# Performance work log

Measured on AMD Instinct MI355X. Metric: run time of the kernel, lower is better.

The kernel has to match this reference:

```python
import jax, jax.numpy as jnp
import numpy as np

B, T, S, D, K = 512, 49, 200, 512, 128


def setup_inputs() -> dict:
    key = jax.random.key(0)
    ks = jax.random.split(key, 8)
    return {
        "ifeature": jax.random.normal(ks[0], (B, T, D), dtype=jnp.float32),
        "tfeature_h": jax.random.normal(ks[1], (B, S, D), dtype=jnp.float32),
        "w_Dense_Vi_0": jax.random.normal(ks[2], (D, K), dtype=jnp.float32) * 0.05,
        "w_Dense_Vt_0": jax.random.normal(ks[3], (D, K), dtype=jnp.float32) * 0.05,
        "w_Dense_Pi_0": jax.random.normal(ks[4], (2 * K, 1), dtype=jnp.float32) * 0.05,
        "b_Dense_Pi_0": jnp.zeros((T,), dtype=jnp.float32),
        "w_Dense_Vi_1": jax.random.normal(ks[5], (D, K), dtype=jnp.float32) * 0.05,
        "w_Dense_Vt_1": jax.random.normal(ks[6], (D, K), dtype=jnp.float32) * 0.05,
        "w_Dense_Pi_1": jax.random.normal(ks[7], (2 * K, 1), dtype=jnp.float32) * 0.05,
        "b_Dense_Pi_1": jnp.zeros((S,), dtype=jnp.float32),
    }


def reference(ifeature, tfeature_h, w_Dense_Vi_0, w_Dense_Vt_0, w_Dense_Pi_0,
              b_Dense_Pi_0, w_Dense_Vi_1, w_Dense_Vt_1, w_Dense_Pi_1, b_Dense_Pi_1):
    # tfeature: mean-pooled text, [B, D]
    tfeature = jnp.mean(tfeature_h, axis=1)

    # --- attention over image regions (title_len) ---
    w_Vi_0 = jnp.einsum('btd,dk->btk', ifeature, w_Dense_Vi_0)          # [B,T,K]
    w_Vt_0 = (tfeature @ w_Dense_Vt_0)[:, None, :]                      # [B,1,K] broadcast to T
    Hi = jnp.tanh(jnp.concatenate(
        [w_Vi_0, jnp.broadcast_to(w_Vt_0, w_Vi_0.shape)], axis=-1))     # [B,T,2K]
    Hi_w_b = jnp.einsum('btk,k->bt', Hi, w_Dense_Pi_0[:, 0]) + b_Dense_Pi_0
    Pi = jax.nn.softmax(Hi_w_b, axis=-1)                                # [B,T]
    Vi = jnp.einsum('bt,btd->bd', Pi, ifeature)                         # attended image feature

    # --- attention over text tokens (seq_len) ---
    w_Vi_1 = (Vi @ w_Dense_Vi_1)[:, None, :]                            # [B,1,K]
    w_Vt_1 = jnp.einsum('bsd,dk->bsk', tfeature_h, w_Dense_Vt_1)        # [B,S,K]
    Ht = jnp.tanh(jnp.concatenate(
        [jnp.broadcast_to(w_Vi_1, w_Vt_1.shape), w_Vt_1], axis=-1))     # [B,S,2K]
    Ht_b = jnp.einsum('bsk,k->bs', Ht, w_Dense_Pi_1[:, 0]) + b_Dense_Pi_1
    Pt = jax.nn.softmax(Ht_b, axis=-1)                                  # [B,S]

    # NOTE: original call() returns Pt_Vt (weighted tokens), not the pooled Vt.
    Pt_Vt = Pt[:, :, None] * tfeature_h                                 # [B,S,D]
    return Pt_Vt
```

## Files before the change

kernel.cpp:

```cpp
#include <hip/hip_runtime.h>
#include <math.h>

#define BB 512
#define SS 200
#define DD 512
#define KK 128
#define RR (BB * SS)

typedef __attribute__((ext_vector_type(8))) short bf16x8;
typedef __attribute__((ext_vector_type(4))) float f32x4;

__device__ inline unsigned short f2bf(float f) {
    union { float f; unsigned int u; } v; v.f = f;
    unsigned int r = v.u + 0x7FFFu + ((v.u >> 16) & 1u);
    return (unsigned short)(r >> 16);
}

__device__ inline bf16x8 pack8(const float4& a, const float4& b) {
    bf16x8 p;
    p[0] = (short)f2bf(a.x); p[1] = (short)f2bf(a.y);
    p[2] = (short)f2bf(a.z); p[3] = (short)f2bf(a.w);
    p[4] = (short)f2bf(b.x); p[5] = (short)f2bf(b.y);
    p[6] = (short)f2bf(b.z); p[7] = (short)f2bf(b.w);
    return p;
}

__device__ inline float fast_tanh(float x) {
    x = fminf(10.f, fmaxf(-10.f, x));
    float t = exp2f(x * 2.885390081777927f);
    return (t - 1.f) * __builtin_amdgcn_rcpf(t + 1.f);
}

__global__ void wt_kernel(const float* __restrict__ W, unsigned short* __restrict__ Wt2) {
    int i = blockIdx.x * 256 + threadIdx.x;
    int j = i & 7;
    int l = (i >> 3) & 63;
    int n = (i >> 9) & 7;
    int t = i >> 12;
    int k = n * 16 + (l & 15);
    int d = t * 32 + (l >> 4) * 8 + j;
    Wt2[i] = f2bf(W[d * KK + k]);
}

__global__ __launch_bounds__(256, 3) void logits_kernel(
    const float* __restrict__ tfh,
    const unsigned short* __restrict__ Wt2,
    const float* __restrict__ wpk,
    const float* __restrict__ bias,
    float* __restrict__ logits)
{
    int tid = threadIdx.x;
    int w   = tid >> 6;
    int l   = tid & 63;
    int l15 = l & 15;
    int g   = l >> 4;
    int W   = blockIdx.x * 4 + w;
    int row = W * 16 + l15;

    const float* a = tfh + (size_t)row * DD + g * 8;
    const unsigned short* bp = Wt2 + (size_t)l * 8;

    bf16x8 abf[16];
    #pragma unroll
    for (int t = 0; t < 16; ++t) {
        float4 v0 = *(const float4*)(a + t * 32);
        float4 v1 = *(const float4*)(a + t * 32 + 4);
        abf[t] = pack8(v0, v1);
    }

    f32x4 acc[8];
    #pragma unroll
    for (int n = 0; n < 8; ++n) acc[n] = (f32x4){0.f, 0.f, 0.f, 0.f};

    #pragma unroll
    for (int t = 0; t < 16; ++t) {
        const unsigned short* bt = bp + (size_t)t * (8 * 64 * 8);
        #pragma unroll
        for (int n = 0; n < 8; ++n) {
            bf16x8 bf = *(const bf16x8*)(bt + n * 512);
            acc[n] = __builtin_amdgcn_mfma_f32_16x16x32_bf16(abf[t], bf, acc[n], 0, 0, 0);
        }
    }

    float wv[8];
    #pragma unroll
    for (int n = 0; n < 8; ++n) wv[n] = wpk[n * 16 + l15];

    float rs[4];
    #pragma unroll
    for (int r = 0; r < 4; ++r) rs[r] = 0.f;
    #pragma unroll
    for (int n = 0; n < 8; ++n)
        #pragma unroll
        for (int r = 0; r < 4; ++r)
            rs[r] += fast_tanh(acc[n][r]) * wv[n];
    #pragma unroll
    for (int r = 0; r < 4; ++r) {
        float v = rs[r];
        v += __shfl_xor(v, 1, 64);
        v += __shfl_xor(v, 2, 64);
        v += __shfl_xor(v, 4, 64);
        v += __shfl_xor(v, 8, 64);
        rs[r] = v;
    }
    if (l15 == 0) {
        #pragma unroll
        for (int r = 0; r < 4; ++r) {
            int grow = W * 16 + g * 4 + r;
            logits[grow] = rs[r] + bias[grow % SS];
        }
    }
}

__global__ __launch_bounds__(1024) void softmax_mul_kernel(
    const float* __restrict__ logits,
    const float* __restrict__ tfh,
    float* __restrict__ out)
{
    int b = blockIdx.x;
    int tid = threadIdx.x;
    __shared__ float Pt[SS];
    __shared__ float wpart[16];

    float v = (tid < SS) ? logits[(size_t)b * SS + tid] : -INFINITY;
    float m = v;
    #pragma unroll
    for (int off = 32; off > 0; off >>= 1) m = fmaxf(m, __shfl_xor(m, off, 64));
    if ((tid & 63) == 0) wpart[tid >> 6] = m;
    __syncthreads();
    m = -INFINITY;
    #pragma unroll
    for (int i = 0; i < 16; ++i) m = fmaxf(m, wpart[i]);
    float e = (tid < SS) ? expf(v - m) : 0.f;
    float ssum = e;
    #pragma unroll
    for (int off = 32; off > 0; off >>= 1) ssum += __shfl_xor(ssum, off, 64);
    __syncthreads();
    if ((tid & 63) == 0) wpart[tid >> 6] = ssum;
    __syncthreads();
    ssum = 0.f;
    #pragma unroll
    for (int i = 0; i < 16; ++i) ssum += wpart[i];
    if (tid < SS) Pt[tid] = e / ssum;
    __syncthreads();

    const f32x4* src = (const f32x4*)(tfh + (size_t)b * SS * DD);
    f32x4*       dst = (f32x4*)(out + (size_t)b * SS * DD);
    const int n4 = SS * DD / 4;
    for (int i = tid; i < n4; i += 1024) {
        float p = Pt[i >> 7];
        f32x4 x = src[i];
        x = x * p;
        __builtin_nontemporal_store(x, dst + i);
    }
}

extern "C" void kernel_launch(void* const* d_in, const int* in_sizes, int n_in,
                              void* d_out, int out_size, void* d_ws, size_t ws_size,
                              hipStream_t stream) {
    const float* tfh   = (const float*)d_in[1];
    const float* wVt1  = (const float*)d_in[7];
    const float* wp1   = (const float*)d_in[8];
    const float* bias1 = (const float*)d_in[9];
    float* out = (float*)d_out;

    unsigned short* Wt2 = (unsigned short*)d_ws;
    float* logits = (float*)((char*)d_ws + (128 << 10));

    wt_kernel<<<(16 * 8 * 64 * 8) / 256, 256, 0, stream>>>(wVt1, Wt2);
    logits_kernel<<<RR / 64, 256, 0, stream>>>(tfh, Wt2, wp1 + KK, bias1, logits);
    softmax_mul_kernel<<<BB, 1024, 0, stream>>>(logits, tfh, out);
}
```

Measured before the change: 131.2 us.

## Stream A-operand loads per k-step to raise occupancy in logits kernel

Drops the up-front load of all sixteen bf16 A fragments into registers. Each k-step now converts the current chunk and prefetches the next one while its MFMAs run, and the launch bound rises from 3 to 8 blocks per CU. The aim is lower register pressure and more resident waves to hide global-memory latency. The trade-off is far less memory-level parallelism per wave: only one chunk is in flight instead of sixteen, and the outer loop is no longer unrolled.

```diff
diff --git a/kernel.cpp b/kernel.cpp
--- a/kernel.cpp
+++ b/kernel.cpp
@@ -42,7 +42,7 @@
     Wt2[i] = f2bf(W[d * KK + k]);
 }
 
-__global__ __launch_bounds__(256, 3) void logits_kernel(
+__global__ __launch_bounds__(256, 8) void logits_kernel(
     const float* __restrict__ tfh,
     const unsigned short* __restrict__ Wt2,
     const float* __restrict__ wpk,
@@ -54,46 +54,43 @@
     int l   = tid & 63;
     int l15 = l & 15;
     int g   = l >> 4;
-    int W   = blockIdx.x * 4 + w;
-    int row = W * 16 + l15;
+    int Wv  = blockIdx.x * 4 + w;
+    int row = Wv * 16 + l15;
 
     const float* a = tfh + (size_t)row * DD + g * 8;
     const unsigned short* bp = Wt2 + (size_t)l * 8;
-
-    bf16x8 abf[16];
-    #pragma unroll
-    for (int t = 0; t < 16; ++t) {
-        float4 v0 = *(const float4*)(a + t * 32);
-        float4 v1 = *(const float4*)(a + t * 32 + 4);
-        abf[t] = pack8(v0, v1);
-    }
 
     f32x4 acc[8];
     #pragma unroll
     for (int n = 0; n < 8; ++n) acc[n] = (f32x4){0.f, 0.f, 0.f, 0.f};
 
-    #pragma unroll
+    float4 c0 = *(const float4*)(a);
+    float4 c1 = *(const float4*)(a + 4);
+
     for (int t = 0; t < 16; ++t) {
+        bf16x8 af = pack8(c0, c1);
+        if (t < 15) {
+            c0 = *(const float4*)(a + (t + 1) * 32);
+            c1 = *(const float4*)(a + (t + 1) * 32 + 4);
+        }
         const unsigned short* bt = bp + (size_t)t * (8 * 64 * 8);
         #pragma unroll
         for (int n = 0; n < 8; ++n) {
             bf16x8 bf = *(const bf16x8*)(bt + n * 512);
-            acc[n] = __builtin_amdgcn_mfma_f32_16x16x32_bf16(abf[t], bf, acc[n], 0, 0, 0);
+            acc[n] = __builtin_amdgcn_mfma_f32_16x16x32_bf16(af, bf, acc[n], 0, 0, 0);
         }
     }
-
-    float wv[8];
-    #pragma unroll
-    for (int n = 0; n < 8; ++n) wv[n] = wpk[n * 16 + l15];
 
     float rs[4];
     #pragma unroll
     for (int r = 0; r < 4; ++r) rs[r] = 0.f;
     #pragma unroll
-    for (int n = 0; n < 8; ++n)
+    for (int n = 0; n < 8; ++n) {
+        float wv = wpk[n * 16 + l15];
         #pragma unroll
         for (int r = 0; r < 4; ++r)
-            rs[r] += fast_tanh(acc[n][r]) * wv[n];
+            rs[r] += fast_tanh(acc[n][r]) * wv;
+    }
     #pragma unroll
     for (int r = 0; r < 4; ++r) {
         float v = rs[r];
@@ -106,7 +103,7 @@
     if (l15 == 0) {
         #pragma unroll
         for (int r = 0; r < 4; ++r) {
-            int grow = W * 16 + g * 4 + r;
+            int grow = Wv * 16 + g * 4 + r;
             logits[grow] = rs[r] + bias[grow % SS];
         }
     }
```

Result: no change. 130.8 us (-0.3%).

## Split logits GEMM into two N-half passes with LDS-staged weights

Applied to the files above, without the earlier changes.

Replaces the single logits kernel with two launches of a half-width kernel. Each launch covers 64 of the 128 K columns and stages its bf16 weight slice in shared memory instead of reading it from global memory per MFMA. The second launch adds the first launch's partial sums and the bias. This halves accumulator registers and lifts the occupancy cap. In exchange, the 210 MB tfeature_h activation is read and converted to bf16 twice, which adds substantial HBM traffic to a memory-bound pipeline.

```diff
diff --git a/kernel.cpp b/kernel.cpp
--- a/kernel.cpp
+++ b/kernel.cpp
@@ -42,23 +42,35 @@
     Wt2[i] = f2bf(W[d * KK + k]);
 }
 
-__global__ __launch_bounds__(256, 3) void logits_kernel(
+__global__ __launch_bounds__(256) void logits_half_kernel(
     const float* __restrict__ tfh,
     const unsigned short* __restrict__ Wt2,
     const float* __restrict__ wpk,
     const float* __restrict__ bias,
-    float* __restrict__ logits)
+    const float* __restrict__ psum_in,
+    float* __restrict__ out,
+    int n0, int final)
 {
+    __shared__ unsigned short Bs[16 * 4 * 64 * 8];
+
     int tid = threadIdx.x;
     int w   = tid >> 6;
     int l   = tid & 63;
     int l15 = l & 15;
     int g   = l >> 4;
-    int W   = blockIdx.x * 4 + w;
-    int row = W * 16 + l15;
 
+    int bn = tid >> 6;
+    int bl = tid & 63;
+    #pragma unroll
+    for (int t = 0; t < 16; ++t) {
+        size_t gsrc = (((size_t)t * 8 + n0 + bn) * 64 + bl) * 8;
+        *(bf16x8*)&Bs[(((t * 4 + bn) * 64 + bl) * 8)] = *(const bf16x8*)(Wt2 + gsrc);
+    }
+    __syncthreads();
+
+    int Wv  = blockIdx.x * 4 + w;
+    int row = Wv * 16 + l15;
     const float* a = tfh + (size_t)row * DD + g * 8;
-    const unsigned short* bp = Wt2 + (size_t)l * 8;
 
     bf16x8 abf[16];
     #pragma unroll
@@ -68,29 +80,28 @@
         abf[t] = pack8(v0, v1);
     }
 
-    f32x4 acc[8];
+    f32x4 acc[4];
     #pragma unroll
-    for (int n = 0; n < 8; ++n) acc[n] = (f32x4){0.f, 0.f, 0.f, 0.f};
+    for (int n = 0; n < 4; ++n) acc[n] = (f32x4){0.f, 0.f, 0.f, 0.f};
 
     #pragma unroll
     for (int t = 0; t < 16; ++t) {
-        const unsigned short* bt = bp + (size_t)t * (8 * 64 * 8);
         #pragma unroll
-        for (int n = 0; n < 8; ++n) {
-            bf16x8 bf = *(const bf16x8*)(bt + n * 512);
+        for (int n = 0; n < 4; ++n) {
+            bf16x8 bf = *(const bf16x8*)&Bs[((t * 4 + n) * 64 + l) * 8];
             acc[n] = __builtin_amdgcn_mfma_f32_16x16x32_bf16(abf[t], bf, acc[n], 0, 0, 0);
         }
     }
 
-    float wv[8];
+    float wv[4];
     #pragma unroll
-    for (int n = 0; n < 8; ++n) wv[n] = wpk[n * 16 + l15];
+    for (int n = 0; n < 4; ++n) wv[n] = wpk[(n0 + n) * 16 + l15];
 
     float rs[4];
     #pragma unroll
     for (int r = 0; r < 4; ++r) rs[r] = 0.f;
     #pragma unroll
-    for (int n = 0; n < 8; ++n)
+    for (int n = 0; n < 4; ++n)
         #pragma unroll
         for (int r = 0; r < 4; ++r)
             rs[r] += fast_tanh(acc[n][r]) * wv[n];
@@ -106,8 +117,10 @@
     if (l15 == 0) {
         #pragma unroll
         for (int r = 0; r < 4; ++r) {
-            int grow = W * 16 + g * 4 + r;
-            logits[grow] = rs[r] + bias[grow % SS];
+            int grow = Wv * 16 + g * 4 + r;
+            float v = rs[r];
+            if (final) v += psum_in[grow] + bias[grow % SS];
+            out[grow] = v;
         }
     }
 }
@@ -166,8 +179,12 @@
 
     unsigned short* Wt2 = (unsigned short*)d_ws;
     float* logits = (float*)((char*)d_ws + (128 << 10));
+    float* psum   = (float*)((char*)d_ws + (1 << 20));
 
     wt_kernel<<<(16 * 8 * 64 * 8) / 256, 256, 0, stream>>>(wVt1, Wt2);
-    logits_kernel<<<RR / 64, 256, 0, stream>>>(tfh, Wt2, wp1 + KK, bias1, logits);
+    logits_half_kernel<<<RR / 64, 256, 0, stream>>>(
+        tfh, Wt2, wp1 + KK, bias1, nullptr, psum, 0, 0);
+    logits_half_kernel<<<RR / 64, 256, 0, stream>>>(
+        tfh, Wt2, wp1 + KK, bias1, psum, logits, 4, 1);
     softmax_mul_kernel<<<BB, 1024, 0, stream>>>(logits, tfh, out);
 }
```

Measured after the change: 152.3 us. 1.16x slower.
